# Optimization experiments

Hardware: AMD Instinct MI355X
Metric: run time of the kernel (lower is better)

Reference implementation:

```python
import jax, jax.numpy as jnp
import numpy as np
from jax import lax

HEADS = 8

# Haar-lifting 4x4 matrices from nlwt_init / inlwt_init
U1P1 = jnp.array([[-0.5, -0.5, -0.5, 0.5], [0.5, -0.5, 0.5, 0.5], [0.5, 0.5, -0.5, 0.5], [0.5, -0.5, -0.5, -0.5]], jnp.float32)
U2P2 = jnp.array([[-1., 1., 1., -1.], [-1., -1., -1., -1.], [-1., -1., 1., 1.], [1., -1., 1., -1.]], jnp.float32)
P2U2 = jnp.array([[-1., -1., -1., 1.], [1., -1., -1., -1.], [1., -1., 1., 1.], [-1., -1., 1., -1.]], jnp.float32)
P1U1 = jnp.array([[-0.125, 0.125, 0.125, 0.125], [-0.125, -0.125, 0.125, -0.125], [-0.125, 0.125, -0.125, -0.125], [0.125, 0.125, 0.125, -0.125]], jnp.float32)


def conv1x1(x, w):
    # w: [out_ch, in_ch]
    return jnp.einsum('oi,bihw->bohw', w, x)


def dwconv3(x, w):
    # depthwise 3x3, w: [C,1,3,3]
    return lax.conv_general_dilated(x, w, (1, 1), [(1, 1), (1, 1)],
                                    dimension_numbers=('NCHW', 'OIHW', 'NCHW'),
                                    feature_group_count=x.shape[1])


def layernorm_c(x, w, b):
    # WithBias LayerNorm over channel dim (to_3d normalizes last dim == c)
    mu = jnp.mean(x, axis=1, keepdims=True)
    var = jnp.var(x, axis=1, keepdims=True)
    return (x - mu) / jnp.sqrt(var + 1e-5) * w[None, :, None, None] + b[None, :, None, None]


def attention(x, temperature, qkv_w, qkv_dw_w, proj_w):
    b, c, h, w = x.shape
    qkv = dwconv3(conv1x1(x, qkv_w), qkv_dw_w)
    q, k, v = jnp.split(qkv, 3, axis=1)
    hd = lambda t: t.reshape(b, HEADS, c // HEADS, h * w)
    q, k, v = hd(q), hd(k), hd(v)
    q = q / jnp.maximum(jnp.linalg.norm(q, axis=-1, keepdims=True), 1e-12)
    k = k / jnp.maximum(jnp.linalg.norm(k, axis=-1, keepdims=True), 1e-12)
    attn = jax.nn.softmax(jnp.einsum('bhcn,bhdn->bhcd', q, k) * temperature, axis=-1)
    out = jnp.einsum('bhcd,bhdn->bhcn', attn, v).reshape(b, c, h, w)
    return conv1x1(out, proj_w)


def ffn(x, pin_w, dw_w, pout_w):
    y = dwconv3(conv1x1(x, pin_w), dw_w)
    y1, y2 = jnp.split(y, 2, axis=1)
    return conv1x1(jax.nn.gelu(y1, approximate=False) * y2, pout_w)


def tblock(x, ln1_w, ln1_b, temperature, qkv_w, qkv_dw_w, proj_w, ln2_w, ln2_b, pin_w, ffn_dw_w, pout_w):
    x = x + attention(layernorm_c(x, ln1_w, ln1_b), temperature, qkv_w, qkv_dw_w, proj_w)
    x = x + ffn(layernorm_c(x, ln2_w, ln2_b), pin_w, ffn_dw_w, pout_w)
    return x


def nlwt(x):
    # lifting wavelet decompose (nlwt_init), vectorized im2col via reshape
    b, c, h, w = x.shape
    h1, w1 = h // 2, w // 2
    col = x.reshape(b, c, h1, 2, w1, 2).transpose(0, 1, 3, 5, 2, 4).reshape(b, c, 4, h1 * w1)
    x1 = jnp.einsum('ij,bcjn->bcin', U1P1, col).reshape(b, c, 4, h1, w1)
    t1 = x1[:, :, 0]
    t2 = jnp.roll(x1[:, :, 1], -1, axis=2)
    t3 = jnp.roll(x1[:, :, 2], -1, axis=3)
    t4 = jnp.roll(x1[:, :, 3], (-1, -1), axis=(2, 3))
    x1 = jnp.stack([t1, t2, t3, t4], axis=2).reshape(b, c, 4, h1 * w1)
    x2 = jnp.einsum('ij,bcjn->bcin', U2P2, x1).reshape(b, c, 4, h1, w1)
    return x2[:, :, 0], x2[:, :, 1], x2[:, :, 2], x2[:, :, 3]


def inlwt(A, B, C, D):
    # lifting wavelet reconstruct (inlwt_init), vectorized col2im via reshape
    b, c, h1, w1 = A.shape
    Y1 = jnp.stack([A, B, C, D], axis=2).reshape(b, c, 4, h1 * w1)
    Y2 = jnp.einsum('ij,bcjn->bcin', P2U2, Y1).reshape(b, c, 4, h1, w1)
    t1 = Y2[:, :, 0]
    t2 = jnp.roll(Y2[:, :, 1], 1, axis=2)
    t3 = jnp.roll(Y2[:, :, 2], 1, axis=3)
    t4 = jnp.roll(Y2[:, :, 3], (1, 1), axis=(2, 3))
    Y2 = jnp.stack([t1, t2, t3, t4], axis=2).reshape(b, c, 4, h1 * w1)
    Y3 = jnp.einsum('ij,bcjn->bcin', P1U1, Y2).reshape(b, c, 2, 2, h1, w1)
    return Y3.transpose(0, 1, 4, 2, 5, 3).reshape(b, c, 2 * h1, 2 * w1)


def gfm(x1, x2, ca_w1, ca_w2, sa_w, sa_b):
    Cc = x1.shape[1]
    cat = jnp.concatenate([x1, x2], axis=1)  # [b, 2C, h, w]
    avg = jnp.mean(cat, axis=(2, 3), keepdims=True)
    mx = jnp.max(cat, axis=(2, 3), keepdims=True)
    mlp = lambda t: conv1x1(jax.nn.relu(conv1x1(t, ca_w1)), ca_w2)
    cw = jax.nn.sigmoid(mlp(avg) + mlp(mx))  # [b, 2C, 1, 1]
    cw = cw.reshape(-1, 2, Cc)[:, :, :, None, None]
    out = cw[:, 0] * x1 + cw[:, 1] * x2
    savg = jnp.mean(out, axis=1, keepdims=True)
    smax = jnp.max(out, axis=1, keepdims=True)
    sa = lax.conv_general_dilated(jnp.concatenate([savg, smax], axis=1), sa_w, (1, 1), [(3, 3), (3, 3)],
                                  dimension_numbers=('NCHW', 'OIHW', 'NCHW')) + sa_b[None, :, None, None]
    return jax.nn.sigmoid(sa) * out


def setup_inputs() -> dict:
    key = jax.random.key(0)
    ks = jax.random.split(key, 16)
    B, C, H, W = 2, 48, 256, 256
    hidden = int(C * 2.66)  # 127
    s = 0.05
    return {
        'x': jax.random.normal(ks[0], (B, C, H, W), jnp.float32),
        'ln1_w': jnp.ones((C,), jnp.float32),
        'ln1_b': jnp.zeros((C,), jnp.float32),
        'temperature': jnp.ones((HEADS, 1, 1), jnp.float32),
        'qkv_w': jax.random.normal(ks[1], (3 * C, C), jnp.float32) * s,
        'qkv_dw_w': jax.random.normal(ks[2], (3 * C, 1, 3, 3), jnp.float32) * s,
        'proj_w': jax.random.normal(ks[3], (C, C), jnp.float32) * s,
        'ln2_w': jnp.ones((C,), jnp.float32),
        'ln2_b': jnp.zeros((C,), jnp.float32),
        'pin_w': jax.random.normal(ks[4], (2 * hidden, C), jnp.float32) * s,
        'ffn_dw_w': jax.random.normal(ks[5], (2 * hidden, 1, 3, 3), jnp.float32) * s,
        'pout_w': jax.random.normal(ks[6], (C, hidden), jnp.float32) * s,
        'ca_w1': jax.random.normal(ks[7], (2 * C // 16, 2 * C), jnp.float32) * s,
        'ca_w2': jax.random.normal(ks[8], (2 * C, 2 * C // 16), jnp.float32) * s,
        'sa_w': jax.random.normal(ks[9], (1, 2, 7, 7), jnp.float32) * s,
        'sa_b': jnp.zeros((1,), jnp.float32),
    }


def reference(x, ln1_w, ln1_b, temperature, qkv_w, qkv_dw_w, proj_w, ln2_w, ln2_b, pin_w, ffn_dw_w, pout_w, ca_w1, ca_w2, sa_w, sa_b):
    tb = lambda t: tblock(t, ln1_w, ln1_b, temperature, qkv_w, qkv_dw_w, proj_w, ln2_w, ln2_b, pin_w, ffn_dw_w, pout_w)
    branch1 = tb(x)
    A, Bh, Ch, Dh = nlwt(x)
    branch2 = inlwt(tb(A), Bh, Ch, Dh)
    return gfm(branch1, branch2, ca_w1, ca_w2, sa_w, sa_b)
```

## Files before the change

### kernel.cpp

```cpp
#include <hip/hip_runtime.h>
#include <math.h>

namespace {

constexpr int BB   = 2;
constexpr int CC   = 48;
constexpr int NHEAD= 8;
constexpr int CPH  = 6;
constexpr int HID  = 127;
constexpr int QKVC = 144;
constexpr int PINC = 254;
constexpr int N1   = 256*256;
constexpr int N2   = 128*128;
constexpr size_t PS2 = (size_t)BB*CC*N2;
constexpr size_t NB1 = (size_t)BB*CC*N1;

using short8  = __attribute__((ext_vector_type(8))) short;
using floatx4 = __attribute__((ext_vector_type(4))) float;

__device__ __forceinline__ float b2f(unsigned short u) {
    unsigned int x = ((unsigned int)u) << 16;
    float f; __builtin_memcpy(&f, &x, 4); return f;
}
__device__ __forceinline__ unsigned short f2b(float f) {
    unsigned int x; __builtin_memcpy(&x, &f, 4);
    unsigned int r = (x + 0x7FFFu + ((x >> 16) & 1u)) >> 16;
    return (unsigned short)r;
}
__device__ __forceinline__ unsigned int pack2(float lo, float hi) {
    return (unsigned int)f2b(lo) | ((unsigned int)f2b(hi) << 16);
}

__device__ __forceinline__ float gelu_t(float x) {
    float z = 1.5957691216057308f * (x + 0.044715f * x * x * x);
    float e = __expf(z);
    return x * (1.0f - 1.0f / (e + 1.0f));
}

__global__ void k_zero(float* __restrict__ p, int n)
{
    int i = blockIdx.x*256 + threadIdx.x;
    if (i < n) p[i] = 0.f;
}

__global__ void k_repw(const float* __restrict__ w, float* __restrict__ wt, int O, int K)
{
    int i = blockIdx.x*256 + threadIdx.x;
    if (i < O*K) {
        int c = i / O, oc = i - c*O;
        wt[c*O + oc] = w[oc*K + c];
    }
}

template<int OCR, int OCT>
__global__ void k_packw_mfma(const float* __restrict__ w, unsigned short* __restrict__ wf)
{
    int i = blockIdx.x*256 + threadIdx.x;
    if (i >= OCT*2*64) return;
    int lane = i & 63, ts = i >> 6;
    int s = ts & 1, t = ts >> 1;
    int oc = t*16 + (lane & 15);
    int kb = s*32 + (lane >> 4)*8;
    float v[8];
#pragma unroll
    for (int j = 0; j < 8; ++j) {
        int k = kb + j;
        v[j] = (oc < OCR && k < 48) ? w[oc*48 + k] : 0.f;
    }
    uint4 o;
    o.x = pack2(v[0], v[1]); o.y = pack2(v[2], v[3]);
    o.z = pack2(v[4], v[5]); o.w = pack2(v[6], v[7]);
    *(uint4*)(wf + (size_t)i*8) = o;
}

__global__ __launch_bounds__(256) void k_ln_t(const float* __restrict__ X,
                       const float* __restrict__ lw, const float* __restrict__ lb,
                       unsigned short* __restrict__ xh, int Ns)
{
    int g = blockIdx.x*256 + threadIdx.x;
    int half = Ns >> 1;
    int b = g >= half ? 1 : 0;
    int pp = (g - b*half)*2;
    const float* xb = X + (size_t)b*CC*Ns + pp;
    float v0[CC], v1[CC];
    float s0=0.f, s20=0.f, s1=0.f, s21=0.f;
#pragma unroll
    for (int c = 0; c < CC; ++c) {
        float2 v = *(const float2*)(xb + (size_t)c*Ns);
        v0[c]=v.x; v1[c]=v.y;
        s0 += v.x; s20 = fmaf(v.x,v.x,s20);
        s1 += v.y; s21 = fmaf(v.y,v.y,s21);
    }
    float mu0 = s0*(1.0f/CC), mu1 = s1*(1.0f/CC);
    float i0 = 1.0f/sqrtf(s20*(1.0f/CC)-mu0*mu0+1e-5f);
    float i1 = 1.0f/sqrtf(s21*(1.0f/CC)-mu1*mu1+1e-5f);
    unsigned short* r0 = xh + ((size_t)b*Ns + pp)*48;
    unsigned short* r1 = r0 + 48;
#pragma unroll
    for (int j = 0; j < 6; ++j) {
        uint4 o0, o1;
        float y[8], z[8];
#pragma unroll
        for (int e = 0; e < 8; ++e) {
            int c = j*8 + e;
            float w = lw[c], bb2 = lb[c];
            y[e] = (v0[c]-mu0)*i0*w + bb2;
            z[e] = (v1[c]-mu1)*i1*w + bb2;
        }
        o0.x = pack2(y[0],y[1]); o0.y = pack2(y[2],y[3]);
        o0.z = pack2(y[4],y[5]); o0.w = pack2(y[6],y[7]);
        o1.x = pack2(z[0],z[1]); o1.y = pack2(z[2],z[3]);
        o1.z = pack2(z[4],z[5]); o1.w = pack2(z[6],z[7]);
        *(uint4*)(r0 + j*8) = o0;
        *(uint4*)(r1 + j*8) = o1;
    }
}

template<int OCR, int OCT>
__global__ __launch_bounds__(256) void k_conv_mfma(const unsigned short* __restrict__ xh,
                       const unsigned short* __restrict__ wf,
                       unsigned short* __restrict__ out, int Ns)
{
    int wid = (blockIdx.x*256 + (int)threadIdx.x) >> 6;
    int lane = threadIdx.x & 63;
    int tpb = Ns >> 4;
    int b = wid / tpb, pxt = wid - b*tpb;
    int px0 = pxt << 4;
    int col = lane & 15, grp = lane >> 4;
    const unsigned short* xb = xh + ((size_t)b*Ns + px0 + col)*48 + grp*8;
    short8 b0 = *(const short8*)(xb);
    short8 b1 = *(const short8*)(xb + 32);
    unsigned short* ob = out + (size_t)b*OCR*Ns + px0 + col;
    int ocb0 = grp*4;
#pragma unroll
    for (int t = 0; t < OCT; ++t) {
        floatx4 acc = {};
        short8 a0 = *(const short8*)(wf + (size_t)((t*2+0)*64 + lane)*8);
        short8 a1 = *(const short8*)(wf + (size_t)((t*2+1)*64 + lane)*8);
        acc = __builtin_amdgcn_mfma_f32_16x16x32_bf16(a0, b0, acc, 0, 0, 0);
        acc = __builtin_amdgcn_mfma_f32_16x16x32_bf16(a1, b1, acc, 0, 0, 0);
#pragma unroll
        for (int r = 0; r < 4; ++r) {
            int oc = t*16 + ocb0 + r;
            if (OCR % 16 == 0 || oc < OCR)
                ob[(size_t)oc*Ns] = f2b(acc[r]);
        }
    }
}

__device__ __forceinline__ void load_row10(const unsigned short* __restrict__ p,
                                           bool lok, bool rrok, float (&f)[10])
{
    uint4 cv = *(const uint4*)p;
    unsigned int u0=cv.x,u1=cv.y,u2=cv.z,u3=cv.w;
    f[1]=b2f((unsigned short)(u0&0xffffu)); f[2]=b2f((unsigned short)(u0>>16));
    f[3]=b2f((unsigned short)(u1&0xffffu)); f[4]=b2f((unsigned short)(u1>>16));
    f[5]=b2f((unsigned short)(u2&0xffffu)); f[6]=b2f((unsigned short)(u2>>16));
    f[7]=b2f((unsigned short)(u3&0xffffu)); f[8]=b2f((unsigned short)(u3>>16));
    f[0] = lok  ? b2f(p[-1]) : 0.f;
    f[9] = rrok ? b2f(p[8])  : 0.f;
}

__device__ __forceinline__ void dw4x8(const unsigned short* __restrict__ plane,
                                      const float* __restrict__ w9,
                                      int y0, int x0, int Hs, int Ws, float (&acc)[4][8])
{
#pragma unroll
    for (int r = 0; r < 4; ++r)
#pragma unroll
        for (int i = 0; i < 8; ++i) acc[r][i] = 0.f;
    bool lok = x0 > 0, rrok = x0 + 8 < Ws;
#pragma unroll
    for (int ir = 0; ir < 6; ++ir) {
        int r = y0 + ir - 1;
        if (r < 0 || r >= Hs) continue;
        float f[10];
        load_row10(plane + (size_t)r*Ws + x0, lok, rrok, f);
#pragma unroll
        for (int ky = 0; ky < 3; ++ky) {
            int orow = ir - ky;
            if (orow < 0 || orow > 3) continue;
            float w0 = w9[ky*3], w1 = w9[ky*3+1], w2 = w9[ky*3+2];
#pragma unroll
            for (int i = 0; i < 8; ++i)
                acc[orow][i] = fmaf(f[i], w0, fmaf(f[i+1], w1, fmaf(f[i+2], w2, acc[orow][i])));
        }
    }
}

__global__ __launch_bounds__(256) void k_dw3v(const unsigned short* __restrict__ in,
                      const float* __restrict__ w,
                      unsigned short* __restrict__ out, int Hs, int Ws, int lgNgt, int lgWq)
{
    int g = blockIdx.x*256 + threadIdx.x;
    int t = g & ((1<<lgNgt)-1), bc = g >> lgNgt;
    int c = bc % QKVC;
    int y0 = (t >> lgWq) << 2, x0 = (t & ((1<<lgWq)-1)) << 3;
    int Ns = Hs*Ws;
    float acc[4][8];
    dw4x8(in + (size_t)bc*Ns, w + c*9, y0, x0, Hs, Ws, acc);
    unsigned short* ob = out + (size_t)bc*Ns + (size_t)y0*Ws + x0;
#pragma unroll
    for (int r = 0; r < 4; ++r) {
        uint4 o;
        o.x = pack2(acc[r][0],acc[r][1]); o.y = pack2(acc[r][2],acc[r][3]);
        o.z = pack2(acc[r][4],acc[r][5]); o.w = pack2(acc[r][6],acc[r][7]);
        *(uint4*)(ob + (size_t)r*Ws) = o;
    }
}

__global__ __launch_bounds__(256) void k_dwgate(const unsigned short* __restrict__ pin,
                         const float* __restrict__ dww,
                         unsigned short* __restrict__ gate, int Hs, int Ws, int lgNgt, int lgWq)
{
    int g = blockIdx.x*256 + threadIdx.x;
    int t = g & ((1<<lgNgt)-1), bc = g >> lgNgt;
    int b = bc / HID, c = bc - b*HID;
    int y0 = (t >> lgWq) << 2, x0 = (t & ((1<<lgWq)-1)) << 3;
    int Ns = Hs*Ws;
    float a1[4][8], a2[4][8];
    dw4x8(pin + ((size_t)b*PINC + c)*Ns,       dww + c*9,       y0, x0, Hs, Ws, a1);
    dw4x8(pin + ((size_t)b*PINC + HID + c)*Ns, dww + (c+HID)*9, y0, x0, Hs, Ws, a2);
    unsigned short* ob = gate + (size_t)bc*Ns + (size_t)y0*Ws + x0;
#pragma unroll
    for (int r = 0; r < 4; ++r) {
        uint4 o;
        o.x = pack2(gelu_t(a1[r][0])*a2[r][0], gelu_t(a1[r][1])*a2[r][1]);
        o.y = pack2(gelu_t(a1[r][2])*a2[r][2], gelu_t(a1[r][3])*a2[r][3]);
        o.z = pack2(gelu_t(a1[r][4])*a2[r][4], gelu_t(a1[r][5])*a2[r][5]);
        o.w = pack2(gelu_t(a1[r][6])*a2[r][6], gelu_t(a1[r][7])*a2[r][7]);
        *(uint4*)(ob + (size_t)r*Ws) = o;
    }
}

__global__ __launch_bounds__(256) void k_qk_stats(const unsigned short* __restrict__ qkvd,
                                                  float* __restrict__ st, int Ns)
{
    const int NBLK = 32;
    int bh = blockIdx.x / NBLK, blk = blockIdx.x % NBLK;
    int b = bh / NHEAD, h = bh % NHEAD;
    const unsigned short* qb = qkvd + ((size_t)b*QKVC + h*CPH)*Ns;
    const unsigned short* kb = qkvd + ((size_t)b*QKVC + 48 + h*CPH)*Ns;
    float vals[48];
#pragma unroll
    for (int i = 0; i < 48; ++i) vals[i] = 0.f;
    for (int n = blk*512 + (int)threadIdx.x*2; n < Ns; n += NBLK*512) {
        float q0[CPH], q1[CPH], k0[CPH], k1[CPH];
#pragma unroll
        for (int i = 0; i < CPH; ++i) {
            unsigned int qu = *(const unsigned int*)(qb + (size_t)i*Ns + n);
            unsigned int ku = *(const unsigned int*)(kb + (size_t)i*Ns + n);
            q0[i] = b2f((unsigned short)(qu & 0xffffu)); q1[i] = b2f((unsigned short)(qu >> 16));
            k0[i] = b2f((unsigned short)(ku & 0xffffu)); k1[i] = b2f((unsigned short)(ku >> 16));
        }
#pragma unroll
        for (int i = 0; i < CPH; ++i) {
            vals[i]   = fmaf(q0[i],q0[i], fmaf(q1[i],q1[i], vals[i]));
            vals[6+i] = fmaf(k0[i],k0[i], fmaf(k1[i],k1[i], vals[6+i]));
        }
#pragma unroll
        for (int i = 0; i < CPH; ++i)
#pragma unroll
            for (int j = 0; j < CPH; ++j)
                vals[12+i*6+j] = fmaf(q0[i],k0[j], fmaf(q1[i],k1[j], vals[12+i*6+j]));
    }
    __shared__ float red[4][48];
    int lane = threadIdx.x & 63, wave = threadIdx.x >> 6;
#pragma unroll
    for (int i = 0; i < 48; ++i) {
        float v = vals[i];
#pragma unroll
        for (int off = 32; off > 0; off >>= 1) v += __shfl_down(v, off);
        if (lane == 0) red[wave][i] = v;
    }
    __syncthreads();
    if ((int)threadIdx.x < 48) {
        int i = threadIdx.x;
        float v = red[0][i] + red[1][i] + red[2][i] + red[3][i];
        float* dst;
        if (i < 6)       dst = st + b*48 + h*CPH + i;
        else if (i < 12) dst = st + 96 + b*48 + h*CPH + (i-6);
        else             dst = st + 192 + (b*NHEAD+h)*36 + (i-12);
        atomicAdd(dst, v);
    }
}

__global__ void k_attn(const float* __restrict__ st, const float* __restrict__ temp,
                       const float* __restrict__ projw, float* __restrict__ Mt)
{
    int t = threadIdx.x;
    if (t >= BB*NHEAD) return;
    int b = t / NHEAD, h = t % NHEAD;
    const float* sqq = st + b*48 + h*CPH;
    const float* sqk = st + 96 + b*48 + h*CPH;
    const float* g   = st + 192 + (b*NHEAD+h)*36;
    float T = temp[h];
    float nq[CPH], nk[CPH];
#pragma unroll
    for (int i = 0; i < CPH; ++i) {
        nq[i] = fmaxf(sqrtf(sqq[i]), 1e-12f);
        nk[i] = fmaxf(sqrtf(sqk[i]), 1e-12f);
    }
    float a[CPH][CPH];
#pragma unroll
    for (int c = 0; c < CPH; ++c) {
        float l[CPH]; float m = -1e30f;
#pragma unroll
        for (int d = 0; d < CPH; ++d) {
            l[d] = g[c*6+d] / (nq[c]*nk[d]) * T;
            m = fmaxf(m, l[d]);
        }
        float ssum = 0.f;
#pragma unroll
        for (int d = 0; d < CPH; ++d) { l[d] = expf(l[d]-m); ssum += l[d]; }
        float r = 1.0f/ssum;
#pragma unroll
        for (int d = 0; d < CPH; ++d) a[c][d] = l[d]*r;
    }
    float* mb = Mt + b*CC*CC;
#pragma unroll
    for (int d = 0; d < CPH; ++d) {
        for (int oc = 0; oc < CC; ++oc) {
            float m = 0.f;
#pragma unroll
            for (int c = 0; c < CPH; ++c)
                m = fmaf(projw[oc*CC + h*CPH + c], a[c][d], m);
            mb[(h*CPH+d)*CC + oc] = m;
        }
    }
}

__global__ __launch_bounds__(256) void k_av_proj(const unsigned short* __restrict__ qkvd,
                          const float* __restrict__ Mt, const float* __restrict__ X,
                          float* __restrict__ x1, int Ns)
{
    int g = blockIdx.x*256 + threadIdx.x;
    int half = Ns >> 1;
    int b = g >= half ? 1 : 0;
    int pp = (g - b*half)*2;
    int ocb = blockIdx.y * 16;
    const unsigned short* vb = qkvd + ((size_t)b*QKVC + 96)*Ns + pp;
    const float* mt = Mt + b*CC*CC;
    float a0[16], a1[16];
#pragma unroll
    for (int i = 0; i < 16; ++i) { a0[i] = 0.f; a1[i] = 0.f; }
#pragma unroll
    for (int c0 = 0; c0 < CC; c0 += 8) {
        unsigned int gv[8];
#pragma unroll
        for (int u = 0; u < 8; ++u)
            gv[u] = *(const unsigned int*)(vb + (size_t)(c0+u)*Ns);
#pragma unroll
        for (int u = 0; u < 8; ++u) {
            float t0 = b2f((unsigned short)(gv[u] & 0xffffu));
            float t1 = b2f((unsigned short)(gv[u] >> 16));
            const float* wr = mt + (c0+u)*CC + ocb;
#pragma unroll
            for (int i = 0; i < 16; ++i) {
                float w = wr[i];
                a0[i] = fmaf(t0, w, a0[i]);
                a1[i] = fmaf(t1, w, a1[i]);
            }
        }
    }
    const float* xb = X + (size_t)b*CC*Ns + pp;
    float* ob = x1 + (size_t)b*CC*Ns + pp;
#pragma unroll
    for (int i = 0; i < 16; ++i) {
        float2 xv = *(const float2*)(xb + (size_t)(ocb+i)*Ns);
        float2 o; o.x = xv.x + a0[i]; o.y = xv.y + a1[i];
        *(float2*)(ob + (size_t)(ocb+i)*Ns) = o;
    }
}

template<int U>
__device__ __forceinline__ void pout_chunk(const unsigned short* __restrict__ gb, int c0, int Ns,
                                           const float* __restrict__ wt, int ocb,
                                           float (&a0)[16], float (&a1)[16])
{
    unsigned int gv[U];
#pragma unroll
    for (int u = 0; u < U; ++u)
        gv[u] = *(const unsigned int*)(gb + (size_t)(c0+u)*Ns);
#pragma unroll
    for (int u = 0; u < U; ++u) {
        float t0 = b2f((unsigned short)(gv[u] & 0xffffu));
        float t1 = b2f((unsigned short)(gv[u] >> 16));
        const float* wr = wt + (c0+u)*48 + ocb;
#pragma unroll
        for (int i = 0; i < 16; ++i) {
            float w = wr[i];
            a0[i] = fmaf(t0, w, a0[i]);
            a1[i] = fmaf(t1, w, a1[i]);
        }
    }
}

__global__ __launch_bounds__(256) void k_pout(const unsigned short* __restrict__ gate,
                       const float* __restrict__ wt, const float* __restrict__ x1,
                       float* __restrict__ out, int Ns)
{
    int g = blockIdx.x*256 + threadIdx.x;
    int half = Ns >> 1;
    int b = g >= half ? 1 : 0;
    int pp = (g - b*half)*2;
    int ocb = blockIdx.y * 16;
    const unsigned short* gb = gate + (size_t)b*HID*Ns + pp;
    float a0[16], a1[16];
#pragma unroll
    for (int i = 0; i < 16; ++i) { a0[i] = 0.f; a1[i] = 0.f; }
    int c = 0;
    for (; c + 8 <= HID; c += 8)
        pout_chunk<8>(gb, c, Ns, wt, ocb, a0, a1);
    pout_chunk<7>(gb, c, Ns, wt, ocb, a0, a1);
    const float* xb = x1 + (size_t)b*CC*Ns + pp;
    float* ob = out + (size_t)b*CC*Ns + pp;
#pragma unroll
    for (int i = 0; i < 16; ++i) {
        float2 xv = *(const float2*)(xb + (size_t)(ocb+i)*Ns);
        float2 o; o.x = xv.x + a0[i]; o.y = xv.y + a1[i];
        *(float2*)(ob + (size_t)(ocb+i)*Ns) = o;
    }
}

__global__ __launch_bounds__(256) void k_nlwt(const float* __restrict__ X, float* __restrict__ A4)
{
    int g = blockIdx.x*256 + threadIdx.x;
    int n = g & (N2-1); int bc = g >> 14;
    int h1 = n >> 7, w1 = n & 127;
    int hb = (h1+1)&127, wb = (w1+1)&127;
    const float* xp = X + (size_t)bc * N1;
    float t1, t2, t3, t4;
    {
        int y=h1, z=w1;
        float c0=xp[(2*y)*256+2*z], c1=xp[(2*y)*256+2*z+1], c2=xp[(2*y+1)*256+2*z], c3=xp[(2*y+1)*256+2*z+1];
        t1 = 0.5f*(-c0 - c1 - c2 + c3);
    }
    {
        int y=hb, z=w1;
        float c0=xp[(2*y)*256+2*z], c1=xp[(2*y)*256+2*z+1], c2=xp[(2*y+1)*256+2*z], c3=xp[(2*y+1)*256+2*z+1];
        t2 = 0.5f*( c0 - c1 + c2 + c3);
    }
    {
        int y=h1, z=wb;
        float c0=xp[(2*y)*256+2*z], c1=xp[(2*y)*256+2*z+1], c2=xp[(2*y+1)*256+2*z], c3=xp[(2*y+1)*256+2*z+1];
        t3 = 0.5f*( c0 + c1 - c2 + c3);
    }
    {
        int y=hb, z=wb;
        float c0=xp[(2*y)*256+2*z], c1=xp[(2*y)*256+2*z+1], c2=xp[(2*y+1)*256+2*z], c3=xp[(2*y+1)*256+2*z+1];
        t4 = 0.5f*( c0 - c1 - c2 - c3);
    }
    size_t o = (size_t)bc*N2 + n;
    A4[o]           = -t1 + t2 + t3 - t4;
    A4[PS2 + o]     = -t1 - t2 - t3 - t4;
    A4[2*PS2 + o]   = -t1 - t2 + t3 + t4;
    A4[3*PS2 + o]   =  t1 - t2 + t3 - t4;
}

__global__ __launch_bounds__(256) void k_inlwt(const float* __restrict__ Ain, const float* __restrict__ A4,
                        float* __restrict__ out)
{
    int g = blockIdx.x*256 + threadIdx.x;
    int n = g & (N2-1); int bc = g >> 14;
    int h1 = n >> 7, w1 = n & 127;
    int hm = (h1-1)&127, wm = (w1-1)&127;
    const float* I0 = Ain + (size_t)bc*N2;
    const float* I1 = A4 + PS2   + (size_t)bc*N2;
    const float* I2 = A4 + 2*PS2 + (size_t)bc*N2;
    const float* I3 = A4 + 3*PS2 + (size_t)bc*N2;
    int i00 = h1*128+w1, i10 = hm*128+w1, i01 = h1*128+wm, i11 = hm*128+wm;
    float t1, t2, t3, t4;
    { float a=I0[i00], b2=I1[i00], c2=I2[i00], d2=I3[i00]; t1 = -a - b2 - c2 + d2; }
    { float a=I0[i10], b2=I1[i10], c2=I2[i10], d2=I3[i10]; t2 =  a - b2 - c2 - d2; }
    { float a=I0[i01], b2=I1[i01], c2=I2[i01], d2=I3[i01]; t3 =  a - b2 + c2 + d2; }
    { float a=I0[i11], b2=I1[i11], c2=I2[i11], d2=I3[i11]; t4 = -a - b2 + c2 - d2; }
    float y00 = 0.125f*(-t1 + t2 + t3 + t4);
    float y01 = 0.125f*(-t1 - t2 + t3 - t4);
    float y10 = 0.125f*(-t1 + t2 - t3 - t4);
    float y11 = 0.125f*( t1 + t2 + t3 - t4);
    float* ob = out + (size_t)bc * N1;
    int oy = h1*2, ox = w1*2;
    ob[(size_t)oy*256 + ox]       = y00;
    ob[(size_t)oy*256 + ox + 1]   = y01;
    ob[(size_t)(oy+1)*256 + ox]   = y10;
    ob[(size_t)(oy+1)*256 + ox+1] = y11;
}

constexpr int CSEG = 8;
__global__ __launch_bounds__(256) void k_chstat_part(const float* __restrict__ b1, const float* __restrict__ b2,
                         float* __restrict__ ps, float* __restrict__ pm)
{
    int bc = blockIdx.x;
    int seg = blockIdx.y;
    int b = bc / 96, ch = bc % 96;
    const float* src = (ch < 48 ? b1 + ((size_t)b*CC + ch)*N1
                                : b2 + ((size_t)b*CC + (ch-48))*N1) + (size_t)seg*(N1/CSEG);
    const float4* s4 = (const float4*)src;
    float s = 0.f, m = -1e30f;
    for (int i = threadIdx.x; i < N1/CSEG/4; i += 256) {
        float4 v = s4[i];
        s += v.x+v.y+v.z+v.w;
        m = fmaxf(m, fmaxf(fmaxf(v.x,v.y), fmaxf(v.z,v.w)));
    }
    int lane = threadIdx.x & 63, wave = threadIdx.x >> 6;
    __shared__ float rs[4], rm[4];
#pragma unroll
    for (int off = 32; off > 0; off >>= 1) {
        s += __shfl_down(s, off);
        m = fmaxf(m, __shfl_down(m, off));
    }
    if (lane == 0) { rs[wave] = s; rm[wave] = m; }
    __syncthreads();
    if (threadIdx.x == 0) {
        ps[bc*CSEG + seg] = rs[0]+rs[1]+rs[2]+rs[3];
        pm[bc*CSEG + seg] = fmaxf(fmaxf(rm[0],rm[1]), fmaxf(rm[2],rm[3]));
    }
}

__global__ void k_chstat_fin(const float* __restrict__ ps, const float* __restrict__ pm,
                             float* __restrict__ avg, float* __restrict__ mxo)
{
    int t = threadIdx.x;
    if (t >= BB*96) return;
    float s = 0.f, m = -1e30f;
#pragma unroll
    for (int j = 0; j < CSEG; ++j) {
        s += ps[t*CSEG+j];
        m = fmaxf(m, pm[t*CSEG+j]);
    }
    avg[t] = s*(1.0f/N1);
    mxo[t] = m;
}

__global__ void k_cw(const float* __restrict__ avg, const float* __restrict__ mx,
                     const float* __restrict__ w1, const float* __restrict__ w2,
                     float* __restrict__ cw)
{
    int t = threadIdx.x;
    if (t >= BB*96) return;
    int b = t / 96, o = t % 96;
    float ta[6], tm[6];
#pragma unroll
    for (int j = 0; j < 6; ++j) {
        float sa = 0.f, sm = 0.f;
        for (int i = 0; i < 96; ++i) {
            float w = w1[j*96+i];
            sa = fmaf(w, avg[b*96+i], sa);
            sm = fmaf(w, mx[b*96+i], sm);
        }
        ta[j] = sa > 0.f ? sa : 0.f;
        tm[j] = sm > 0.f ? sm : 0.f;
    }
    float ua = 0.f, um = 0.f;
#pragma unroll
    for (int j = 0; j < 6; ++j) {
        ua = fmaf(w2[o*6+j], ta[j], ua);
        um = fmaf(w2[o*6+j], tm[j], um);
    }
    float z = ua + um;
    cw[t] = 1.0f/(1.0f+expf(-z));
}

__global__ __launch_bounds__(256) void k_gfm_out(const float* __restrict__ b1, const float* __restrict__ b2,
                          const float* __restrict__ cw, float* __restrict__ ob,
                          float* __restrict__ savg, float* __restrict__ smax)
{
    int g = blockIdx.x*256 + threadIdx.x;
    int b = g >> 16, p = g & (N1-1);
    float s = 0.f, m = -1e30f;
#pragma unroll
    for (int c = 0; c < CC; ++c) {
        size_t idx = ((size_t)b*CC + c)*N1 + p;
        float o = cw[b*96 + c]*b1[idx] + cw[b*96 + 48 + c]*b2[idx];
        ob[idx] = o;
        s += o; m = fmaxf(m, o);
    }
    savg[(size_t)b*N1 + p] = s*(1.0f/CC);
    smax[(size_t)b*N1 + p] = m;
}

__global__ __launch_bounds__(256) void k_final(const float* __restrict__ savg, const float* __restrict__ smax,
                        const float* __restrict__ saw, const float* __restrict__ sab,
                        const float* __restrict__ ob, float* __restrict__ out)
{
    int g = blockIdx.x*256 + threadIdx.x;
    int b = g >> 16, p = g & (N1-1);
    int y = p >> 8, x = p & 255;
    float s = sab[0];
    const float* av = savg + (size_t)b*N1;
    const float* mx = smax + (size_t)b*N1;
#pragma unroll
    for (int ky = 0; ky < 7; ++ky) {
        int yy = y + ky - 3;
        bool yok = (yy >= 0) && (yy < 256);
        int yc = yy < 0 ? 0 : (yy > 255 ? 255 : yy);
#pragma unroll
        for (int kx = 0; kx < 7; ++kx) {
            int xx = x + kx - 3;
            bool ok = yok && (xx >= 0) && (xx < 256);
            int xc = xx < 0 ? 0 : (xx > 255 ? 255 : xx);
            int idx = yc*256 + xc;
            float a = av[idx], m2 = mx[idx];
            s = fmaf(ok ? a  : 0.f, saw[ky*7+kx], s);
            s = fmaf(ok ? m2 : 0.f, saw[49 + ky*7+kx], s);
        }
    }
    float sig = 1.0f/(1.0f+expf(-s));
#pragma unroll
    for (int c = 0; c < CC; ++c) {
        size_t idx = ((size_t)b*CC + c)*N1 + p;
        out[idx] = sig * ob[idx];
    }
}

__device__ __forceinline__ int ilog2(int v) { return 31 - __builtin_clz(v); }

}

extern "C" void kernel_launch(void* const* d_in, const int* in_sizes, int n_in,
                              void* d_out, int out_size, void* d_ws, size_t ws_size,
                              hipStream_t stream)
{
    const float* x    = (const float*)d_in[0];
    const float* ln1w = (const float*)d_in[1];
    const float* ln1b = (const float*)d_in[2];
    const float* temp = (const float*)d_in[3];
    const float* qkvw = (const float*)d_in[4];
    const float* qkvdw= (const float*)d_in[5];
    const float* projw= (const float*)d_in[6];
    const float* ln2w = (const float*)d_in[7];
    const float* ln2b = (const float*)d_in[8];
    const float* pinw = (const float*)d_in[9];
    const float* ffdw = (const float*)d_in[10];
    const float* poutw= (const float*)d_in[11];
    const float* caw1 = (const float*)d_in[12];
    const float* caw2 = (const float*)d_in[13];
    const float* saw  = (const float*)d_in[14];
    const float* sab  = (const float*)d_in[15];

    float* wsf  = (float*)d_ws;
    float* A4   = wsf;
    float* br1  = A4 + 4*PS2;
    float* br2  = br1 + NB1;
    float* x1b  = br2 + NB1;
    float* tbA  = x1b + NB1;
    float* qkv  = tbA + PS2;
    float* qkvd = qkv + (size_t)BB*QKVC*N1;
    float* stats= qkvd + (size_t)BB*QKVC*N1;
    float* wfqf = stats + 4096;
    float* wfpf = wfqf + 4608;
    float* wor  = wfpf + 8192;
    float* chps = wor + HID*48;
    float* chpm = chps + 192*CSEG;
    float* savg = chpm + 192*CSEG;
    float* smax = savg + (size_t)BB*N1;
    float* Mt   = smax + (size_t)BB*N1;

    unsigned short* wfq = (unsigned short*)wfqf;
    unsigned short* wfp = (unsigned short*)wfpf;

    k_packw_mfma<QKVC, 9><<<(9*2*64+255)/256, 256, 0, stream>>>(qkvw, wfq);
    k_packw_mfma<PINC, 16><<<(16*2*64+255)/256, 256, 0, stream>>>(pinw, wfp);
    k_repw<<<(HID*48+255)/256, 256, 0, stream>>>(poutw, wor, 48, HID);

    auto tb = [&](const float* Xin, float* outp, int Hs, int Ws) {
        int Ns = Hs*Ws;
        int npix = BB*Ns;
        int lgWq = 31 - __builtin_clz(Ws >> 3);
        int lgNgt = (31 - __builtin_clz(Hs >> 2)) + lgWq;
        unsigned short* xhat = (unsigned short*)qkvd;
        k_zero<<<3, 256, 0, stream>>>(stats, 768);
        k_ln_t<<<npix/512, 256, 0, stream>>>(Xin, ln1w, ln1b, xhat, Ns);
        k_conv_mfma<QKVC, 9><<<npix/64, 256, 0, stream>>>(xhat, wfq, (unsigned short*)qkv, Ns);
        k_dw3v<<<(BB*QKVC*(Ns/32))/256, 256, 0, stream>>>((const unsigned short*)qkv, qkvdw,
                                                          (unsigned short*)qkvd, Hs, Ws, lgNgt, lgWq);
        k_qk_stats<<<BB*NHEAD*32, 256, 0, stream>>>((const unsigned short*)qkvd, stats, Ns);
        k_attn<<<1, 64, 0, stream>>>(stats, temp, projw, Mt);
        dim3 g4(npix/512, 3);
        k_av_proj<<<g4, 256, 0, stream>>>((const unsigned short*)qkvd, Mt, Xin, x1b, Ns);
        k_ln_t<<<npix/512, 256, 0, stream>>>(x1b, ln2w, ln2b, xhat, Ns);
        k_conv_mfma<PINC, 16><<<npix/64, 256, 0, stream>>>(xhat, wfp, (unsigned short*)qkv, Ns);
        k_dwgate<<<(BB*HID*(Ns/32)+255)/256, 256, 0, stream>>>((const unsigned short*)qkv, ffdw,
                                                        (unsigned short*)qkvd, Hs, Ws, lgNgt, lgWq);
        dim3 g6(npix/512, 3);
        k_pout<<<g6, 256, 0, stream>>>((const unsigned short*)qkvd, wor, x1b, outp, Ns);
    };

    tb(x, br1, 256, 256);
    k_nlwt<<<(BB*CC*N2)/256, 256, 0, stream>>>(x, A4);
    tb(A4, tbA, 128, 128);
    k_inlwt<<<(BB*CC*N2)/256, 256, 0, stream>>>(tbA, A4, br2);
    dim3 gc(BB*96, CSEG);
    k_chstat_part<<<gc, 256, 0, stream>>>(br1, br2, chps, chpm);
    k_chstat_fin<<<1, 256, 0, stream>>>(chps, chpm, stats + 1344, stats + 1536);
    k_cw<<<1, 256, 0, stream>>>(stats + 1344, stats + 1536, caw1, caw2, stats + 1728);
    k_gfm_out<<<(BB*N1)/256, 256, 0, stream>>>(br1, br2, stats + 1728, x1b, savg, smax);
    k_final<<<(BB*N1)/256, 256, 0, stream>>>(savg, smax, saw, sab, x1b, (float*)d_out);
}
```

Baseline: 437.2 us.

## Shrink depthwise tiles to 2x8 and compute all output channels per pixel in projections

New measurement: 499.3 us. +14.2%, slower.

```diff
diff --git a/kernel.cpp b/kernel.cpp
--- a/kernel.cpp
+++ b/kernel.cpp
@@ -161,17 +161,17 @@
     f[9] = rrok ? b2f(p[8])  : 0.f;
 }
 
-__device__ __forceinline__ void dw4x8(const unsigned short* __restrict__ plane,
+__device__ __forceinline__ void dw2x8(const unsigned short* __restrict__ plane,
                                       const float* __restrict__ w9,
-                                      int y0, int x0, int Hs, int Ws, float (&acc)[4][8])
-{
-#pragma unroll
-    for (int r = 0; r < 4; ++r)
+                                      int y0, int x0, int Hs, int Ws, float (&acc)[2][8])
+{
+#pragma unroll
+    for (int r = 0; r < 2; ++r)
 #pragma unroll
         for (int i = 0; i < 8; ++i) acc[r][i] = 0.f;
     bool lok = x0 > 0, rrok = x0 + 8 < Ws;
 #pragma unroll
-    for (int ir = 0; ir < 6; ++ir) {
+    for (int ir = 0; ir < 4; ++ir) {
         int r = y0 + ir - 1;
         if (r < 0 || r >= Hs) continue;
         float f[10];
@@ -179,7 +179,7 @@
 #pragma unroll
         for (int ky = 0; ky < 3; ++ky) {
             int orow = ir - ky;
-            if (orow < 0 || orow > 3) continue;
+            if (orow < 0 || orow > 1) continue;
             float w0 = w9[ky*3], w1 = w9[ky*3+1], w2 = w9[ky*3+2];
 #pragma unroll
             for (int i = 0; i < 8; ++i)
@@ -195,13 +195,13 @@
     int g = blockIdx.x*256 + threadIdx.x;
     int t = g & ((1<<lgNgt)-1), bc = g >> lgNgt;
     int c = bc % QKVC;
-    int y0 = (t >> lgWq) << 2, x0 = (t & ((1<<lgWq)-1)) << 3;
+    int y0 = (t >> lgWq) << 1, x0 = (t & ((1<<lgWq)-1)) << 3;
     int Ns = Hs*Ws;
-    float acc[4][8];
-    dw4x8(in + (size_t)bc*Ns, w + c*9, y0, x0, Hs, Ws, acc);
+    float acc[2][8];
+    dw2x8(in + (size_t)bc*Ns, w + c*9, y0, x0, Hs, Ws, acc);
     unsigned short* ob = out + (size_t)bc*Ns + (size_t)y0*Ws + x0;
 #pragma unroll
-    for (int r = 0; r < 4; ++r) {
+    for (int r = 0; r < 2; ++r) {
         uint4 o;
         o.x = pack2(acc[r][0],acc[r][1]); o.y = pack2(acc[r][2],acc[r][3]);
         o.z = pack2(acc[r][4],acc[r][5]); o.w = pack2(acc[r][6],acc[r][7]);
@@ -216,14 +216,14 @@
     int g = blockIdx.x*256 + threadIdx.x;
     int t = g & ((1<<lgNgt)-1), bc = g >> lgNgt;
     int b = bc / HID, c = bc - b*HID;
-    int y0 = (t >> lgWq) << 2, x0 = (t & ((1<<lgWq)-1)) << 3;
+    int y0 = (t >> lgWq) << 1, x0 = (t & ((1<<lgWq)-1)) << 3;
     int Ns = Hs*Ws;
-    float a1[4][8], a2[4][8];
-    dw4x8(pin + ((size_t)b*PINC + c)*Ns,       dww + c*9,       y0, x0, Hs, Ws, a1);
-    dw4x8(pin + ((size_t)b*PINC + HID + c)*Ns, dww + (c+HID)*9, y0, x0, Hs, Ws, a2);
+    float a1[2][8], a2[2][8];
+    dw2x8(pin + ((size_t)b*PINC + c)*Ns,       dww + c*9,       y0, x0, Hs, Ws, a1);
+    dw2x8(pin + ((size_t)b*PINC + HID + c)*Ns, dww + (c+HID)*9, y0, x0, Hs, Ws, a2);
     unsigned short* ob = gate + (size_t)bc*Ns + (size_t)y0*Ws + x0;
 #pragma unroll
-    for (int r = 0; r < 4; ++r) {
+    for (int r = 0; r < 2; ++r) {
         uint4 o;
         o.x = pack2(gelu_t(a1[r][0])*a2[r][0], gelu_t(a1[r][1])*a2[r][1]);
         o.y = pack2(gelu_t(a1[r][2])*a2[r][2], gelu_t(a1[r][3])*a2[r][3]);
@@ -335,64 +335,50 @@
                           float* __restrict__ x1, int Ns)
 {
     int g = blockIdx.x*256 + threadIdx.x;
-    int half = Ns >> 1;
-    int b = g >= half ? 1 : 0;
-    int pp = (g - b*half)*2;
-    int ocb = blockIdx.y * 16;
-    const unsigned short* vb = qkvd + ((size_t)b*QKVC + 96)*Ns + pp;
+    int b = g >= Ns ? 1 : 0;
+    int px = g - b*Ns;
+    const unsigned short* vb = qkvd + ((size_t)b*QKVC + 96)*Ns + px;
     const float* mt = Mt + b*CC*CC;
-    float a0[16], a1[16];
-#pragma unroll
-    for (int i = 0; i < 16; ++i) { a0[i] = 0.f; a1[i] = 0.f; }
+    float a[CC];
+#pragma unroll
+    for (int i = 0; i < CC; ++i) a[i] = 0.f;
 #pragma unroll
     for (int c0 = 0; c0 < CC; c0 += 8) {
-        unsigned int gv[8];
+        unsigned short gv[8];
 #pragma unroll
         for (int u = 0; u < 8; ++u)
-            gv[u] = *(const unsigned int*)(vb + (size_t)(c0+u)*Ns);
+            gv[u] = vb[(size_t)(c0+u)*Ns];
 #pragma unroll
         for (int u = 0; u < 8; ++u) {
-            float t0 = b2f((unsigned short)(gv[u] & 0xffffu));
-            float t1 = b2f((unsigned short)(gv[u] >> 16));
-            const float* wr = mt + (c0+u)*CC + ocb;
-#pragma unroll
-            for (int i = 0; i < 16; ++i) {
-                float w = wr[i];
-                a0[i] = fmaf(t0, w, a0[i]);
-                a1[i] = fmaf(t1, w, a1[i]);
-            }
-        }
-    }
-    const float* xb = X + (size_t)b*CC*Ns + pp;
-    float* ob = x1 + (size_t)b*CC*Ns + pp;
-#pragma unroll
-    for (int i = 0; i < 16; ++i) {
-        float2 xv = *(const float2*)(xb + (size_t)(ocb+i)*Ns);
-        float2 o; o.x = xv.x + a0[i]; o.y = xv.y + a1[i];
-        *(float2*)(ob + (size_t)(ocb+i)*Ns) = o;
-    }
+            float tv = b2f(gv[u]);
+            const float* wr = mt + (c0+u)*CC;
+#pragma unroll
+            for (int i = 0; i < CC; ++i)
+                a[i] = fmaf(tv, wr[i], a[i]);
+        }
+    }
+    const float* xb = X + (size_t)b*CC*Ns + px;
+    float* ob = x1 + (size_t)b*CC*Ns + px;
+#pragma unroll
+    for (int i = 0; i < CC; ++i)
+        ob[(size_t)i*Ns] = xb[(size_t)i*Ns] + a[i];
 }
 
 template<int U>
-__device__ __forceinline__ void pout_chunk(const unsigned short* __restrict__ gb, int c0, int Ns,
-                                           const float* __restrict__ wt, int ocb,
-                                           float (&a0)[16], float (&a1)[16])
-{
-    unsigned int gv[U];
+__device__ __forceinline__ void pout1_chunk(const unsigned short* __restrict__ gb, int c0, int Ns,
+                                            const float* __restrict__ wt, float (&a)[CC])
+{
+    unsigned short gv[U];
 #pragma unroll
     for (int u = 0; u < U; ++u)
-        gv[u] = *(const unsigned int*)(gb + (size_t)(c0+u)*Ns);
+        gv[u] = gb[(size_t)(c0+u)*Ns];
 #pragma unroll
     for (int u = 0; u < U; ++u) {
-        float t0 = b2f((unsigned short)(gv[u] & 0xffffu));
-        float t1 = b2f((unsigned short)(gv[u] >> 16));
-        const float* wr = wt + (c0+u)*48 + ocb;
-#pragma unroll
-        for (int i = 0; i < 16; ++i) {
-            float w = wr[i];
-            a0[i] = fmaf(t0, w, a0[i]);
-            a1[i] = fmaf(t1, w, a1[i]);
-        }
+        float tv = b2f(gv[u]);
+        const float* wr = wt + (c0+u)*CC;
+#pragma unroll
+        for (int i = 0; i < CC; ++i)
+            a[i] = fmaf(tv, wr[i], a[i]);
     }
 }
 
@@ -401,26 +387,21 @@
                        float* __restrict__ out, int Ns)
 {
     int g = blockIdx.x*256 + threadIdx.x;
-    int half = Ns >> 1;
-    int b = g >= half ? 1 : 0;
-    int pp = (g - b*half)*2;
-    int ocb = blockIdx.y * 16;
-    const unsigned short* gb = gate + (size_t)b*HID*Ns + pp;
-    float a0[16], a1[16];
-#pragma unroll
-    for (int i = 0; i < 16; ++i) { a0[i] = 0.f; a1[i] = 0.f; }
+    int b = g >= Ns ? 1 : 0;
+    int px = g - b*Ns;
+    const unsigned short* gb = gate + (size_t)b*HID*Ns + px;
+    float a[CC];
+#pragma unroll
+    for (int i = 0; i < CC; ++i) a[i] = 0.f;
     int c = 0;
     for (; c + 8 <= HID; c += 8)
-        pout_chunk<8>(gb, c, Ns, wt, ocb, a0, a1);
-    pout_chunk<7>(gb, c, Ns, wt, ocb, a0, a1);
-    const float* xb = x1 + (size_t)b*CC*Ns + pp;
-    float* ob = out + (size_t)b*CC*Ns + pp;
-#pragma unroll
-    for (int i = 0; i < 16; ++i) {
-        float2 xv = *(const float2*)(xb + (size_t)(ocb+i)*Ns);
-        float2 o; o.x = xv.x + a0[i]; o.y = xv.y + a1[i];
-        *(float2*)(ob + (size_t)(ocb+i)*Ns) = o;
-    }
+        pout1_chunk<8>(gb, c, Ns, wt, a);
+    pout1_chunk<7>(gb, c, Ns, wt, a);
+    const float* xb = x1 + (size_t)b*CC*Ns + px;
+    float* ob = out + (size_t)b*CC*Ns + px;
+#pragma unroll
+    for (int i = 0; i < CC; ++i)
+        ob[(size_t)i*Ns] = xb[(size_t)i*Ns] + a[i];
 }
 
 __global__ __launch_bounds__(256) void k_nlwt(const float* __restrict__ X, float* __restrict__ A4)
@@ -614,8 +595,6 @@
     }
 }
 
-__device__ __forceinline__ int ilog2(int v) { return 31 - __builtin_clz(v); }
-
 }
 
 extern "C" void kernel_launch(void* const* d_in, const int* in_sizes, int n_in,
@@ -668,23 +647,21 @@
         int Ns = Hs*Ws;
         int npix = BB*Ns;
         int lgWq = 31 - __builtin_clz(Ws >> 3);
-        int lgNgt = (31 - __builtin_clz(Hs >> 2)) + lgWq;
+        int lgNgt = (31 - __builtin_clz(Hs >> 1)) + lgWq;
         unsigned short* xhat = (unsigned short*)qkvd;
         k_zero<<<3, 256, 0, stream>>>(stats, 768);
         k_ln_t<<<npix/512, 256, 0, stream>>>(Xin, ln1w, ln1b, xhat, Ns);
         k_conv_mfma<QKVC, 9><<<npix/64, 256, 0, stream>>>(xhat, wfq, (unsigned short*)qkv, Ns);
-        k_dw3v<<<(BB*QKVC*(Ns/32))/256, 256, 0, stream>>>((const unsigned short*)qkv, qkvdw,
+        k_dw3v<<<(BB*QKVC*(Ns/16))/256, 256, 0, stream>>>((const unsigned short*)qkv, qkvdw,
                                                           (unsigned short*)qkvd, Hs, Ws, lgNgt, lgWq);
         k_qk_stats<<<BB*NHEAD*32, 256, 0, stream>>>((const unsigned short*)qkvd, stats, Ns);
         k_attn<<<1, 64, 0, stream>>>(stats, temp, projw, Mt);
-        dim3 g4(npix/512, 3);
-        k_av_proj<<<g4, 256, 0, stream>>>((const unsigned short*)qkvd, Mt, Xin, x1b, Ns);
+        k_av_proj<<<npix/256, 256, 0, stream>>>((const unsigned short*)qkvd, Mt, Xin, x1b, Ns);
         k_ln_t<<<npix/512, 256, 0, stream>>>(x1b, ln2w, ln2b, xhat, Ns);
         k_conv_mfma<PINC, 16><<<npix/64, 256, 0, stream>>>(xhat, wfp, (unsigned short*)qkv, Ns);
-        k_dwgate<<<(BB*HID*(Ns/32)+255)/256, 256, 0, stream>>>((const unsigned short*)qkv, ffdw,
+        k_dwgate<<<(BB*HID*(Ns/16)+255)/256, 256, 0, stream>>>((const unsigned short*)qkv, ffdw,
                                                         (unsigned short*)qkvd, Hs, Ws, lgNgt, lgWq);
-        dim3 g6(npix/512, 3);
-        k_pout<<<g6, 256, 0, stream>>>((const unsigned short*)qkvd, wor, x1b, outp, Ns);
+        k_pout<<<npix/256, 256, 0, stream>>>((const unsigned short*)qkvd, wor, x1b, outp, Ns);
     };
 
     tb(x, br1, 256, 256);
```
